# Optimization experiments

Measured on AMD Instinct MI355X. Metric: run time of the kernel, lower is better.

The kernel has to match this reference:

```python
import jax, jax.numpy as jnp
import numpy as np

EPS = 1e-5
H, D = 8, 64  # n_heads, head_n_channels


def _instance_norm(x):
    # x: [B, H, N, D]; InstanceNorm1d over grid axis N per (batch, head, channel)
    m = jnp.mean(x, axis=2, keepdims=True)
    v = jnp.var(x, axis=2, keepdims=True)
    return (x - m) * jax.lax.rsqrt(v + EPS)


def setup_inputs() -> dict:
    key = jax.random.key(0)
    ks = jax.random.split(key, 7)
    B, N, C, OUT = 4, 16384, 256, 256
    u_src = jax.random.normal(ks[0], (B, N, C), jnp.float32)
    pos_src = jax.random.uniform(ks[1], (B, N, 2), jnp.float32)
    s_in = 1.0 / np.sqrt(C)
    Wq = jax.random.normal(ks[2], (H * D, C), jnp.float32) * s_in
    Wk = jax.random.normal(ks[3], (H * D, C), jnp.float32) * s_in
    Wv = jax.random.normal(ks[4], (H * D, C), jnp.float32) * s_in
    Wo = jax.random.normal(ks[5], (OUT, H * D), jnp.float32) * (1.0 / np.sqrt(H * D))
    bo = jnp.zeros((OUT,), jnp.float32)
    return {"u_src": u_src, "pos_src": pos_src, "Wq": Wq, "Wk": Wk, "Wv": Wv, "Wo": Wo, "bo": bo}


def reference(u_src, pos_src, Wq, Wk, Wv, Wo, bo):
    B, N, C = u_src.shape
    # q/k/v projections -> [B, H, N, D]
    q = (u_src @ Wq.T).reshape(B, N, H, D).transpose(0, 2, 1, 3)
    k = (u_src @ Wk.T).reshape(B, N, H, D).transpose(0, 2, 1, 3)
    v = (u_src @ Wv.T).reshape(B, N, H, D).transpose(0, 2, 1, 3)
    # instance-norm k, v over the grid (domain) axis
    k = _instance_norm(k)
    v = _instance_norm(v)
    # associative linear attention with uniform quadrature weights 1/N
    w = 1.0 / N
    kv = jnp.einsum('bhnd,bhne->bhde', k, v * w)   # [B,H,D,D]
    u = jnp.einsum('bhnd,bhde->bhne', q, kv)       # [B,H,N,D]
    u = u.transpose(0, 2, 1, 3).reshape(B, N, H * D)
    return u @ Wo.T + bo
```

## Files before the change

kernel.cpp:

```cpp
#include <hip/hip_runtime.h>
#include <hip/hip_bf16.h>

#define BB    4
#define NTOT  16384
#define CC    256
#define HH    8
#define DD    64
#define HD    512
#define OUTC  256

typedef unsigned short u16;
typedef unsigned int u32;
typedef __attribute__((ext_vector_type(8))) short bf16x8;
typedef __attribute__((ext_vector_type(4))) float f32x4;
typedef __attribute__((ext_vector_type(4))) short u16x4;
typedef __attribute__((ext_vector_type(4))) u32 u32x4;

__device__ __forceinline__ float b2f(u16 u) {
    union { float f; u32 i; } x; x.i = ((u32)u) << 16; return x.f;
}
__device__ __forceinline__ u16 f2b(float f) {
    union { float f; u32 i; } x; x.f = f;
    u32 r = x.i + 0x7fffu + ((x.i >> 16) & 1u);
    return (u16)(r >> 16);
}

#define GLD(gp, lp) __builtin_amdgcn_global_load_lds( \
    (const __attribute__((address_space(1))) void*)(gp), \
    (__attribute__((address_space(3))) void*)(lp), 16, 0, 0)

#define MFMA(a, b, c) __builtin_amdgcn_mfma_f32_16x16x32_bf16((a), (b), (c), 0, 0, 0)

__global__ __launch_bounds__(256) void wcvt(
    const float* __restrict__ Wq, const float* __restrict__ Wk,
    const float* __restrict__ Wv, const float* __restrict__ Wo,
    u16* __restrict__ q, u16* __restrict__ k,
    u16* __restrict__ v, u16* __restrict__ o)
{
    const int z = blockIdx.z;
    const float* src = z == 0 ? Wq : z == 1 ? Wk : z == 2 ? Wv : Wo;
    u16* dst = z == 0 ? q : z == 1 ? k : z == 2 ? v : o;
    const int i = (blockIdx.x * 256 + threadIdx.x) * 8;
    const float4 a = *(const float4*)(src + i);
    const float4 b = *(const float4*)(src + i + 4);
    union { bf16x8 v; u16 s[8]; } w;
    w.s[0] = f2b(a.x); w.s[1] = f2b(a.y); w.s[2] = f2b(a.z); w.s[3] = f2b(a.w);
    w.s[4] = f2b(b.x); w.s[5] = f2b(b.y); w.s[6] = f2b(b.z); w.s[7] = f2b(b.w);
    *(bf16x8*)(dst + i) = w.v;
}

__global__ __launch_bounds__(512) void ggemm(
    const float* __restrict__ u, float* __restrict__ Gp, float* __restrict__ suP,
    u16* __restrict__ u_b)
{
    __shared__ u32 Ts[2 * 4640];
    const int z = blockIdx.x, b = z >> 6, ck = z & 63;
    const float* base = u + (long long)b * NTOT * CC + (long long)ck * 256 * CC;
    u16* ub_base = u_b + (long long)b * NTOT * CC + (long long)ck * 256 * CC;
    const int t = threadIdx.x, w = t >> 6, l = t & 63;
    const int wy = w >> 1, wx = w & 1;
    const int r16 = l & 15, quad = l >> 4;
    const int sp = t >> 5;
    const int sq = t & 31;

    const int csa0 = 9 * ((wy * 64 + r16) >> 3) + (r16 & 7);
    const int csb0 = 9 * ((wx * 128 + r16) >> 3) + (r16 & 7);
    const int pr0 = 4 * quad * 290;

    f32x4 acc[4][8] = {};
    float su8[8] = {};

    float4 a0, a1, b0, b1;
    {
        const float* src = base + (long long)(2 * sp) * CC + sq * 8;
        a0 = *(const float4*)src;       a1 = *(const float4*)(src + 4);
        b0 = *(const float4*)(src + CC); b1 = *(const float4*)(src + CC + 4);
    }

    int cur = 0;
    for (int it = 0; it < 8; it++) {
        const u32 coff = cur * 4640;
        {
            union { bf16x8 v; u16 q[8]; } ra, rb;
            ra.q[0] = f2b(a0.x); ra.q[1] = f2b(a0.y); ra.q[2] = f2b(a0.z); ra.q[3] = f2b(a0.w);
            ra.q[4] = f2b(a1.x); ra.q[5] = f2b(a1.y); ra.q[6] = f2b(a1.z); ra.q[7] = f2b(a1.w);
            rb.q[0] = f2b(b0.x); rb.q[1] = f2b(b0.y); rb.q[2] = f2b(b0.z); rb.q[3] = f2b(b0.w);
            rb.q[4] = f2b(b1.x); rb.q[5] = f2b(b1.y); rb.q[6] = f2b(b1.z); rb.q[7] = f2b(b1.w);
#pragma unroll
            for (int k = 0; k < 8; k++)
                su8[k] += b2f(ra.q[k]) + b2f(rb.q[k]);
            u32 pk[8];
#pragma unroll
            for (int k = 0; k < 8; k++)
                pk[k] = (u32)ra.q[k] | ((u32)rb.q[k] << 16);
            u32* dst = Ts + coff + sp * 290 + 9 * sq;
#pragma unroll
            for (int k = 0; k < 8; k++) dst[k] = pk[k];
            {
                u16* ub = ub_base + (long long)(it * 32 + 2 * sp) * CC + sq * 8;
                *(bf16x8*)ub = ra.v;
                *(bf16x8*)(ub + CC) = rb.v;
            }
        }
        __syncthreads();

        if (it < 7) {
            const float* src = base + (long long)((it + 1) * 32 + 2 * sp) * CC + sq * 8;
            a0 = *(const float4*)src;       a1 = *(const float4*)(src + 4);
            b0 = *(const float4*)(src + CC); b1 = *(const float4*)(src + CC + 4);
        }

        bf16x8 a[4], bb[8];
#pragma unroll
        for (int i = 0; i < 4; i++) {
            const int cs = coff + pr0 + csa0 + 18 * i;
            union { u32x4 u4; bf16x8 h; } f;
            f.u4[0] = Ts[cs];       f.u4[1] = Ts[290 + cs];
            f.u4[2] = Ts[580 + cs]; f.u4[3] = Ts[870 + cs];
            a[i] = f.h;
        }
#pragma unroll
        for (int j = 0; j < 8; j++) {
            const int cs = coff + pr0 + csb0 + 18 * j;
            union { u32x4 u4; bf16x8 h; } f;
            f.u4[0] = Ts[cs];       f.u4[1] = Ts[290 + cs];
            f.u4[2] = Ts[580 + cs]; f.u4[3] = Ts[870 + cs];
            bb[j] = f.h;
        }
#pragma unroll
        for (int i = 0; i < 4; i++)
#pragma unroll
            for (int j = 0; j < 8; j++)
                acc[i][j] = MFMA(a[i], bb[j], acc[i][j]);
        cur ^= 1;
    }

    float* Cp = Gp + (long long)z * 65536;
#pragma unroll
    for (int i = 0; i < 4; i++)
#pragma unroll
        for (int j = 0; j < 8; j++)
#pragma unroll
            for (int rr = 0; rr < 4; rr++)
                Cp[(wy * 64 + 16 * i + quad * 4 + rr) * 256 + wx * 128 + 16 * j + r16]
                    = acc[i][j][rr];

    __syncthreads();
    float* S = (float*)Ts;
#pragma unroll
    for (int k = 0; k < 8; k++) S[sp * 264 + sq * 8 + k] = su8[k];
    __syncthreads();
    if (t < 256) {
        float s = 0.f;
#pragma unroll
        for (int p = 0; p < 16; p++) s += S[p * 264 + t];
        suP[z * 256 + t] = s;
    }
}

__global__ __launch_bounds__(256) void gred(
    const float* __restrict__ Gp, const float* __restrict__ suP,
    u16* __restrict__ Gb, float* __restrict__ su)
{
    const int b = blockIdx.y, t = threadIdx.x;
    const int row = blockIdx.x * 4 + (t >> 6);
    const int col = (t & 63) * 4;
    const float* p = Gp + (long long)(b * 64) * 65536 + row * 256 + col;
    f32x4 s = {};
#pragma unroll
    for (int ck = 0; ck < 64; ck++) {
        f32x4 v = *(const f32x4*)(p + (long long)ck * 65536);
        s[0] += v[0]; s[1] += v[1]; s[2] += v[2]; s[3] += v[3];
    }
    union { u16x4 v; u16 q[4]; } pk;
#pragma unroll
    for (int k = 0; k < 4; k++) pk.q[k] = f2b(s[k]);
    *(u16x4*)(Gb + (long long)b * 65536 + row * 256 + col) = pk.v;

    if (blockIdx.x == 0) {
        float s2 = 0.f;
#pragma unroll
        for (int ck = 0; ck < 64; ck++) s2 += suP[(b * 64 + ck) * 256 + t];
        su[b * 256 + t] = s2;
    }
}

__global__ __launch_bounds__(256) void skvz(
    const u16* __restrict__ P2, const float* __restrict__ su,
    const u16* __restrict__ Wk_b, const u16* __restrict__ Wv_b,
    const u16* __restrict__ Wq_b, u16* __restrict__ Zt)
{
    __shared__ u16 pool[20480];
    __shared__ float mkL[64], rkL[64], mvL[64], rvL[64];

    const int bx = blockIdx.x, b = bx >> 3, h = bx & 7;
    const int t = threadIdx.x, w = t >> 6, l = t & 63;
    const int r16 = l & 15, quad = l >> 4;

    const u16* WkH = Wk_b + (h * 64) * 256;
    const u16* WvH = Wv_b + (h * 64) * 256;
    const u16* PkH = P2 + (long long)b * 262144 + (h * 64) * 256;
    const u16* PvH = P2 + (long long)b * 262144 + (512 + h * 64) * 256;

    {
        const int row = t >> 1, half = t & 1;
        const u16* Prow = (row < 64 ? PkH + row * 256 : PvH + (row - 64) * 256) + half * 128;
        const u16* Wrow = (row < 64 ? WkH + row * 256 : WvH + (row - 64) * 256) + half * 128;
        const float* suB = su + b * 256 + half * 128;
        float e2 = 0.f, m = 0.f;
#pragma unroll
        for (int c8 = 0; c8 < 16; c8++) {
            bf16x8 pw = *(const bf16x8*)(Prow + c8 * 8);
            bf16x8 ww = *(const bf16x8*)(Wrow + c8 * 8);
#pragma unroll
            for (int k = 0; k < 8; k++) {
                const float wv_ = b2f((u16)ww[k]);
                e2 += b2f((u16)pw[k]) * wv_;
                m  += wv_ * suB[c8 * 8 + k];
            }
        }
        e2 += __shfl_xor(e2, 1);
        m  += __shfl_xor(m, 1);
        if (half == 0) {
            m *= (1.0f / NTOT);
            const float r = rsqrtf(e2 * (1.0f / NTOT) - m * m + 1e-5f);
            if (row < 64) { mkL[row] = m; rkL[row] = r; }
            else          { mvL[row - 64] = m; rvL[row - 64] = r; }
        }
    }
    __syncthreads();

    const int mh = (w >> 1) * 32, nh = (w & 1) * 32;
    float mkR[2][4], rkR[2][4], mvR[2], rvR[2];
#pragma unroll
    for (int i = 0; i < 2; i++)
#pragma unroll
        for (int rr = 0; rr < 4; rr++) {
            mkR[i][rr] = mkL[mh + 16 * i + quad * 4 + rr];
            rkR[i][rr] = rkL[mh + 16 * i + quad * 4 + rr];
        }
#pragma unroll
    for (int j = 0; j < 2; j++) {
        mvR[j] = mvL[nh + 16 * j + r16];
        rvR[j] = rvL[nh + 16 * j + r16];
    }

    f32x4 accs[2][2] = {};
    for (int ch = 0; ch < 8; ch++) {
        const int ko = quad * 8;
        bf16x8 ap[2], bv[2];
#pragma unroll
        for (int i = 0; i < 2; i++)
            ap[i] = *(const bf16x8*)(PkH + (mh + 16 * i + r16) * 256 + ch * 32 + ko);
#pragma unroll
        for (int j = 0; j < 2; j++)
            bv[j] = *(const bf16x8*)(WvH + (nh + 16 * j + r16) * 256 + ch * 32 + ko);
#pragma unroll
        for (int i = 0; i < 2; i++)
#pragma unroll
            for (int j = 0; j < 2; j++)
                accs[i][j] = MFMA(ap[i], bv[j], accs[i][j]);
    }

    u16* kvTL = pool;
    u16* WqTL = pool + 4096;
#pragma unroll
    for (int i = 0; i < 2; i++)
#pragma unroll
        for (int j = 0; j < 2; j++)
#pragma unroll
            for (int rr = 0; rr < 4; rr++) {
                const int d = mh + 16 * i + quad * 4 + rr;
                const int e = nh + 16 * j + r16;
                const float kv = rkR[i][rr] * rvR[j] *
                    (accs[i][j][rr] * (1.0f / NTOT) - mkR[i][rr] * mvR[j]);
                kvTL[(d >> 5) * 2048 + e * 32 + (d & 31)] = f2b(kv);
            }
    {
        const int d = t >> 2, q = t & 3;
        const u16* Wrow = Wq_b + (h * 64 + d) * 256 + q * 64;
#pragma unroll
        for (int s = 0; s < 8; s++) {
            bf16x8 raw = *(const bf16x8*)(Wrow + s * 8);
#pragma unroll
            for (int k = 0; k < 8; k++) {
                const int c = q * 64 + s * 8 + k;
                WqTL[(d >> 5) * 8192 + c * 32 + (d & 31)] = (u16)raw[k];
            }
        }
    }
    __syncthreads();

    f32x4 accy[4][4] = {};
#pragma unroll
    for (int ch = 0; ch < 2; ch++) {
        const int ko = quad * 8;
        bf16x8 akv[4], bq[4];
#pragma unroll
        for (int i = 0; i < 4; i++)
            akv[i] = *(const bf16x8*)(kvTL + ch * 2048 + (16 * i + r16) * 32 + ko);
#pragma unroll
        for (int j = 0; j < 4; j++)
            bq[j] = *(const bf16x8*)(WqTL + ch * 8192 + (w * 64 + 16 * j + r16) * 32 + ko);
#pragma unroll
        for (int i = 0; i < 4; i++)
#pragma unroll
            for (int j = 0; j < 4; j++)
                accy[i][j] = MFMA(akv[i], bq[j], accy[i][j]);
    }
#pragma unroll
    for (int i = 0; i < 4; i++)
#pragma unroll
        for (int j = 0; j < 4; j++) {
            const int c = w * 64 + 16 * j + r16;
            const int e0 = 16 * i + quad * 4;
            union { u16x4 v; u16 s[4]; } pk;
#pragma unroll
            for (int rr = 0; rr < 4; rr++) pk.s[rr] = f2b(accy[i][j][rr]);
            *(u16x4*)(Zt + ((long long)(b * 256 + c)) * 512 + h * 64 + e0) = pk.v;
        }
}

template <typename CT>
__global__ __launch_bounds__(256) void gemm_bt(
    const u16* __restrict__ A, const u16* __restrict__ Bm,
    CT* __restrict__ C, const float* __restrict__ bias,
    int K, int lda, int ldc,
    long long aStride, long long bStride, long long cStride)
{
    __shared__ u16 As[2][128 * 32];
    __shared__ u16 Bs[2][128 * 32];

    const int bz = blockIdx.z;
    A  += (long long)bz * aStride;
    Bm += (long long)bz * bStride;
    C  += (long long)bz * cStride;

    const int m0 = blockIdx.x * 128;
    const int n0 = blockIdx.y * 128;
    const int t  = threadIdx.x;
    const int wv = t >> 6, l = t & 63;
    const int wy = wv >> 1, wx = wv & 1;
    const int r16  = l & 15;
    const int quad = l >> 4;
    const int srow = wv * 16 + (l >> 2);
    const int scol = (l & 3) * 8;

    auto stage = [&](int kk, int buf) {
#pragma unroll
        for (int s = 0; s < 2; s++) {
            GLD(A + (long long)(m0 + s * 64 + srow) * lda + kk + scol,
                As[buf] + s * 2048 + wv * 512);
            GLD(Bm + (long long)(n0 + s * 64 + srow) * K + kk + scol,
                Bs[buf] + s * 2048 + wv * 512);
        }
    };

    f32x4 acc[4][4] = {};

    stage(0, 0);
    __syncthreads();
    int cur = 0;
    for (int kk = 0; kk < K; kk += 32) {
        if (kk + 32 < K) stage(kk + 32, cur ^ 1);

        bf16x8 a[4], b[4];
#pragma unroll
        for (int i = 0; i < 4; i++)
            a[i] = *(const bf16x8*)(As[cur] + (wy * 64 + 16 * i + r16) * 32 + quad * 8);
#pragma unroll
        for (int j = 0; j < 4; j++)
            b[j] = *(const bf16x8*)(Bs[cur] + (wx * 64 + 16 * j + r16) * 32 + quad * 8);
#pragma unroll
        for (int i = 0; i < 4; i++)
#pragma unroll
            for (int j = 0; j < 4; j++)
                acc[i][j] = MFMA(a[i], b[j], acc[i][j]);
        __syncthreads();
        cur ^= 1;
    }

#pragma unroll
    for (int j = 0; j < 4; j++) {
        const int col = n0 + wx * 64 + 16 * j + r16;
        const float bv = bias ? bias[col] : 0.0f;
#pragma unroll
        for (int i = 0; i < 4; i++) {
#pragma unroll
            for (int r = 0; r < 4; r++) {
                const int row = m0 + wy * 64 + 16 * i + quad * 4 + r;
                const float v = acc[i][j][r] + bv;
                if constexpr (sizeof(CT) == 2) C[(long long)row * ldc + col] = f2b(v);
                else                           C[(long long)row * ldc + col] = v;
            }
        }
    }
}

__global__ __launch_bounds__(256) void gemm_out(
    const u16* __restrict__ Au, const u16* __restrict__ Ft,
    float* __restrict__ C, const float* __restrict__ bias)
{
    __shared__ u16 As[2][128 * 32];
    __shared__ u16 Bs[2][256 * 32];

    const int b = blockIdx.z;
    Au += (long long)b * NTOT * CC;
    const u16* Bm = Ft + (long long)b * 65536;
    C += (long long)b * NTOT * OUTC;

    const int m0 = blockIdx.x * 128;
    const int t  = threadIdx.x;
    const int wv = t >> 6, l = t & 63;
    const int wy = wv >> 1, wx = wv & 1;
    const int r16  = l & 15;
    const int quad = l >> 4;
    const int srow = wv * 16 + (l >> 2);
    const int scol = (l & 3) * 8;

    auto stage = [&](int kk, int buf) {
#pragma unroll
        for (int s = 0; s < 2; s++)
            GLD(Au + (long long)(m0 + s * 64 + srow) * CC + kk + scol,
                As[buf] + s * 2048 + wv * 512);
#pragma unroll
        for (int s = 0; s < 4; s++)
            GLD(Bm + (long long)(s * 64 + srow) * 256 + kk + scol,
                Bs[buf] + s * 2048 + wv * 512);
    };

    f32x4 acc[4][8] = {};

    stage(0, 0);
    __syncthreads();
    int cur = 0;
    for (int kk = 0; kk < 256; kk += 32) {
        if (kk + 32 < 256) stage(kk + 32, cur ^ 1);

        bf16x8 a[4], bb[8];
#pragma unroll
        for (int i = 0; i < 4; i++)
            a[i] = *(const bf16x8*)(As[cur] + (wy * 64 + 16 * i + r16) * 32 + quad * 8);
#pragma unroll
        for (int j = 0; j < 8; j++)
            bb[j] = *(const bf16x8*)(Bs[cur] + (wx * 128 + 16 * j + r16) * 32 + quad * 8);
#pragma unroll
        for (int i = 0; i < 4; i++)
#pragma unroll
            for (int j = 0; j < 8; j++)
                acc[i][j] = MFMA(a[i], bb[j], acc[i][j]);
        __syncthreads();
        cur ^= 1;
    }

#pragma unroll
    for (int j = 0; j < 8; j++) {
        const int col = wx * 128 + 16 * j + r16;
        const float bv = bias[col];
#pragma unroll
        for (int i = 0; i < 4; i++) {
#pragma unroll
            for (int r = 0; r < 4; r++) {
                const int row = m0 + wy * 64 + 16 * i + quad * 4 + r;
                C[(long long)row * OUTC + col] = acc[i][j][r] + bv;
            }
        }
    }
}

extern "C" void kernel_launch(void* const* d_in, const int* in_sizes, int n_in,
                              void* d_out, int out_size, void* d_ws, size_t ws_size,
                              hipStream_t stream)
{
    const float* u_src = (const float*)d_in[0];
    const float* Wq = (const float*)d_in[2];
    const float* Wk = (const float*)d_in[3];
    const float* Wv = (const float*)d_in[4];
    const float* Wo = (const float*)d_in[5];
    const float* bo = (const float*)d_in[6];
    float* out = (float*)d_out;

    char* ws = (char*)d_ws;
    size_t off = 0;
    float* Gp  = (float*)(ws + off); off += 67108864;
    float* suP = (float*)(ws + off); off += 262144;
    u16*  Gb   = (u16*)(ws + off);  off += 524288;
    u16*  Wq_b = (u16*)(ws + off);  off += 262144;
    u16*  Wk_b = (u16*)(ws + off);  off += 262144;
    u16*  Wv_b = (u16*)(ws + off);  off += 262144;
    u16*  Wo_b = (u16*)(ws + off);  off += 262144;
    float* su  = (float*)(ws + off); off += 4096;
    u16*  Zt   = (u16*)(ws + off);  off += 1048576;
    u16*  Ft   = (u16*)(ws + off);  off += 524288;
    u16*  P2   = (u16*)(ws + off);  off += 2097152;
    u16*  u_b  = (u16*)(ws + off);  off += 33554432;

    const dim3 blk(256);

    wcvt<<<dim3(64, 1, 4), blk, 0, stream>>>(Wq, Wk, Wv, Wo, Wq_b, Wk_b, Wv_b, Wo_b);

    ggemm<<<dim3(BB * 64), dim3(512), 0, stream>>>(u_src, Gp, suP, u_b);
    gred<<<dim3(64, BB), blk, 0, stream>>>(Gp, suP, Gb, su);

    gemm_bt<u16><<<dim3(8, 2, BB), blk, 0, stream>>>(
        Wk_b, Gb, P2, nullptr, 256, 256, 256, 0, 65536, 262144);

    skvz<<<dim3(BB * HH), blk, 0, stream>>>(P2, su, Wk_b, Wv_b, Wq_b, Zt);

    gemm_bt<u16><<<dim3(2, 2, BB), blk, 0, stream>>>(
        Wo_b, Zt, Ft, nullptr, 512, 512, 256, 0, 131072, 65536);

    gemm_out<<<dim3(128, 1, BB), blk, 0, stream>>>(u_b, Ft, out, bo);
}
```

Measured before the change: 219.5 us.

## Split Gram GEMM into two row-half blocks of 256 threads

The Gram-matrix kernel now launches 512 blocks of 256 threads instead of 256 blocks of 512 threads. Each block computes one 128-row half of the 256x256 partial Gram tile, and only half 0 writes the bf16 copy of u and the column sums. The shared-memory double buffer is replaced by a single buffer with two barriers per iteration. The aim is more blocks to fill the CUs. The cost is that every input chunk is loaded and converted twice, and load/compute overlap through the second buffer is lost.

```diff
diff --git a/kernel.cpp b/kernel.cpp
--- a/kernel.cpp
+++ b/kernel.cpp
@@ -49,71 +49,84 @@
     *(bf16x8*)(dst + i) = w.v;
 }
 
-__global__ __launch_bounds__(512) void ggemm(
+__global__ __launch_bounds__(256) void ggemm(
     const float* __restrict__ u, float* __restrict__ Gp, float* __restrict__ suP,
     u16* __restrict__ u_b)
 {
-    __shared__ u32 Ts[2 * 4640];
-    const int z = blockIdx.x, b = z >> 6, ck = z & 63;
+    __shared__ u32 Ts[16 * 290];
+    const int z = blockIdx.x;
+    const int half = z >> 8;
+    const int cg = z & 255;
+    const int b = cg >> 6, ck = cg & 63;
     const float* base = u + (long long)b * NTOT * CC + (long long)ck * 256 * CC;
     u16* ub_base = u_b + (long long)b * NTOT * CC + (long long)ck * 256 * CC;
     const int t = threadIdx.x, w = t >> 6, l = t & 63;
     const int wy = w >> 1, wx = w & 1;
     const int r16 = l & 15, quad = l >> 4;
-    const int sp = t >> 5;
+    const int sp0 = t >> 5;
     const int sq = t & 31;
 
-    const int csa0 = 9 * ((wy * 64 + r16) >> 3) + (r16 & 7);
+    const int csa0 = 9 * ((half * 128 + wy * 64 + r16) >> 3) + (r16 & 7);
     const int csb0 = 9 * ((wx * 128 + r16) >> 3) + (r16 & 7);
     const int pr0 = 4 * quad * 290;
 
     f32x4 acc[4][8] = {};
     float su8[8] = {};
 
-    float4 a0, a1, b0, b1;
+    float4 a0, a1, b0, b1, c0, c1, d0, d1;
     {
-        const float* src = base + (long long)(2 * sp) * CC + sq * 8;
-        a0 = *(const float4*)src;       a1 = *(const float4*)(src + 4);
-        b0 = *(const float4*)(src + CC); b1 = *(const float4*)(src + CC + 4);
-    }
-
-    int cur = 0;
+        const float* s1 = base + (long long)(2 * sp0) * CC + sq * 8;
+        const float* s2 = base + (long long)(2 * sp0 + 16) * CC + sq * 8;
+        a0 = *(const float4*)s1;        a1 = *(const float4*)(s1 + 4);
+        b0 = *(const float4*)(s1 + CC); b1 = *(const float4*)(s1 + CC + 4);
+        c0 = *(const float4*)s2;        c1 = *(const float4*)(s2 + 4);
+        d0 = *(const float4*)(s2 + CC); d1 = *(const float4*)(s2 + CC + 4);
+    }
+
     for (int it = 0; it < 8; it++) {
-        const u32 coff = cur * 4640;
+        __syncthreads();
         {
-            union { bf16x8 v; u16 q[8]; } ra, rb;
+            union { bf16x8 v; u16 q[8]; } ra, rb, rc, rd;
             ra.q[0] = f2b(a0.x); ra.q[1] = f2b(a0.y); ra.q[2] = f2b(a0.z); ra.q[3] = f2b(a0.w);
             ra.q[4] = f2b(a1.x); ra.q[5] = f2b(a1.y); ra.q[6] = f2b(a1.z); ra.q[7] = f2b(a1.w);
             rb.q[0] = f2b(b0.x); rb.q[1] = f2b(b0.y); rb.q[2] = f2b(b0.z); rb.q[3] = f2b(b0.w);
             rb.q[4] = f2b(b1.x); rb.q[5] = f2b(b1.y); rb.q[6] = f2b(b1.z); rb.q[7] = f2b(b1.w);
-#pragma unroll
-            for (int k = 0; k < 8; k++)
-                su8[k] += b2f(ra.q[k]) + b2f(rb.q[k]);
-            u32 pk[8];
-#pragma unroll
-            for (int k = 0; k < 8; k++)
-                pk[k] = (u32)ra.q[k] | ((u32)rb.q[k] << 16);
-            u32* dst = Ts + coff + sp * 290 + 9 * sq;
-#pragma unroll
-            for (int k = 0; k < 8; k++) dst[k] = pk[k];
-            {
-                u16* ub = ub_base + (long long)(it * 32 + 2 * sp) * CC + sq * 8;
+            rc.q[0] = f2b(c0.x); rc.q[1] = f2b(c0.y); rc.q[2] = f2b(c0.z); rc.q[3] = f2b(c0.w);
+            rc.q[4] = f2b(c1.x); rc.q[5] = f2b(c1.y); rc.q[6] = f2b(c1.z); rc.q[7] = f2b(c1.w);
+            rd.q[0] = f2b(d0.x); rd.q[1] = f2b(d0.y); rd.q[2] = f2b(d0.z); rd.q[3] = f2b(d0.w);
+            rd.q[4] = f2b(d1.x); rd.q[5] = f2b(d1.y); rd.q[6] = f2b(d1.z); rd.q[7] = f2b(d1.w);
+            u32* dst1 = Ts + sp0 * 290 + 9 * sq;
+            u32* dst2 = Ts + (sp0 + 8) * 290 + 9 * sq;
+#pragma unroll
+            for (int k = 0; k < 8; k++) {
+                dst1[k] = (u32)ra.q[k] | ((u32)rb.q[k] << 16);
+                dst2[k] = (u32)rc.q[k] | ((u32)rd.q[k] << 16);
+            }
+            if (half == 0) {
+#pragma unroll
+                for (int k = 0; k < 8; k++)
+                    su8[k] += (b2f(ra.q[k]) + b2f(rb.q[k])) + (b2f(rc.q[k]) + b2f(rd.q[k]));
+                u16* ub = ub_base + (long long)(it * 32 + 2 * sp0) * CC + sq * 8;
                 *(bf16x8*)ub = ra.v;
                 *(bf16x8*)(ub + CC) = rb.v;
-            }
+                *(bf16x8*)(ub + 16 * CC) = rc.v;
+                *(bf16x8*)(ub + 17 * CC) = rd.v;
+            }
+        }
+        if (it < 7) {
+            const float* s1 = base + (long long)((it + 1) * 32 + 2 * sp0) * CC + sq * 8;
+            const float* s2 = s1 + 16 * CC;
+            a0 = *(const float4*)s1;        a1 = *(const float4*)(s1 + 4);
+            b0 = *(const float4*)(s1 + CC); b1 = *(const float4*)(s1 + CC + 4);
+            c0 = *(const float4*)s2;        c1 = *(const float4*)(s2 + 4);
+            d0 = *(const float4*)(s2 + CC); d1 = *(const float4*)(s2 + CC + 4);
         }
         __syncthreads();
 
-        if (it < 7) {
-            const float* src = base + (long long)((it + 1) * 32 + 2 * sp) * CC + sq * 8;
-            a0 = *(const float4*)src;       a1 = *(const float4*)(src + 4);
-            b0 = *(const float4*)(src + CC); b1 = *(const float4*)(src + CC + 4);
-        }
-
         bf16x8 a[4], bb[8];
 #pragma unroll
         for (int i = 0; i < 4; i++) {
-            const int cs = coff + pr0 + csa0 + 18 * i;
+            const int cs = pr0 + csa0 + 18 * i;
             union { u32x4 u4; bf16x8 h; } f;
             f.u4[0] = Ts[cs];       f.u4[1] = Ts[290 + cs];
             f.u4[2] = Ts[580 + cs]; f.u4[3] = Ts[870 + cs];
@@ -121,7 +134,7 @@
         }
 #pragma unroll
         for (int j = 0; j < 8; j++) {
-            const int cs = coff + pr0 + csb0 + 18 * j;
+            const int cs = pr0 + csb0 + 18 * j;
             union { u32x4 u4; bf16x8 h; } f;
             f.u4[0] = Ts[cs];       f.u4[1] = Ts[290 + cs];
             f.u4[2] = Ts[580 + cs]; f.u4[3] = Ts[870 + cs];
@@ -132,29 +145,28 @@
 #pragma unroll
             for (int j = 0; j < 8; j++)
                 acc[i][j] = MFMA(a[i], bb[j], acc[i][j]);
-        cur ^= 1;
-    }
-
-    float* Cp = Gp + (long long)z * 65536;
+    }
+
+    float* Cp = Gp + (long long)cg * 65536;
 #pragma unroll
     for (int i = 0; i < 4; i++)
 #pragma unroll
         for (int j = 0; j < 8; j++)
 #pragma unroll
             for (int rr = 0; rr < 4; rr++)
-                Cp[(wy * 64 + 16 * i + quad * 4 + rr) * 256 + wx * 128 + 16 * j + r16]
-                    = acc[i][j][rr];
-
-    __syncthreads();
-    float* S = (float*)Ts;
-#pragma unroll
-    for (int k = 0; k < 8; k++) S[sp * 264 + sq * 8 + k] = su8[k];
-    __syncthreads();
-    if (t < 256) {
+                Cp[(half * 128 + wy * 64 + 16 * i + quad * 4 + rr) * 256
+                   + wx * 128 + 16 * j + r16] = acc[i][j][rr];
+
+    if (half == 0) {
+        __syncthreads();
+        float* S = (float*)Ts;
+#pragma unroll
+        for (int k = 0; k < 8; k++) S[sp0 * 264 + sq * 8 + k] = su8[k];
+        __syncthreads();
         float s = 0.f;
 #pragma unroll
-        for (int p = 0; p < 16; p++) s += S[p * 264 + t];
-        suP[z * 256 + t] = s;
+        for (int p = 0; p < 8; p++) s += S[p * 264 + t];
+        suP[cg * 256 + t] = s;
     }
 }
 
@@ -499,7 +511,7 @@
 
     wcvt<<<dim3(64, 1, 4), blk, 0, stream>>>(Wq, Wk, Wv, Wo, Wq_b, Wk_b, Wv_b, Wo_b);
 
-    ggemm<<<dim3(BB * 64), dim3(512), 0, stream>>>(u_src, Gp, suP, u_b);
+    ggemm<<<dim3(512), blk, 0, stream>>>(u_src, Gp, suP, u_b);
     gred<<<dim3(64, BB), blk, 0, stream>>>(Gp, suP, Gb, su);
 
     gemm_bt<u16><<<dim3(8, 2, BB), blk, 0, stream>>>(
```

After: 232.4 us. 1.06x slower.
